# Kernel tuning notes

Hardware: AMD Instinct MI355X
Metric: run time of the kernel (lower is better)

The kernel has to match this reference:

```python
import jax, jax.numpy as jnp
import numpy as np

PI = float(np.pi)


def setup_inputs() -> dict:
    key = jax.random.key(0)
    k1, k2 = jax.random.split(key)
    src = jax.random.normal(k1, (32, 4, 512, 512), dtype=jnp.float32)
    fc2 = jax.random.normal(k2, (32, 7), dtype=jnp.float32)
    return {"src": src, "fc2": fc2}


def _build_mat(fc2):
    # Parameter extraction exactly as in the torch module.
    theta = jnp.clip(fc2[:, 0] * 0.3, -1.0, 1.0) * PI          # rotation angle
    scale = jnp.clip(fc2[:, 1:3] * 0.3 + 1.0, 0.0, 5.0)
    trans = fc2[:, 3:5] * 0.3
    shear = jnp.clip(fc2[:, 5:7] * 0.3, -1.0, 1.0) * PI
    sx, sy = scale[:, 0], scale[:, 1]
    tx, ty = trans[:, 0], trans[:, 1]
    shxy, shyx = shear[:, 0], shear[:, 1]
    c, s = jnp.cos(theta), jnp.sin(theta)
    z, o = jnp.zeros_like(c), jnp.ones_like(c)

    def m3(rows):  # rows: list of 3 lists of 3 (B,) scalars -> (B,3,3)
        return jnp.stack([jnp.stack(r, axis=-1) for r in rows], axis=-2)

    # Note: the torch code stacks rows at dim=2 (making the transpose) then
    # transposes (1,2) back, so the effective matrices are the ones as-written.
    rot = m3([[c, -s, z], [s, c, z], [z, z, o]])
    scl = m3([[sx, z, z], [z, sy, z], [z, z, o]])
    shr = m3([[o, shxy, z], [shyx, o, z], [z, z, o]])
    trn = m3([[o, z, tx], [z, o, ty], [z, z, o]])
    # mat = T @ Sh @ S @ R  (batched 3x3 matmuls)
    return trn @ shr @ scl @ rot


def _affine_grid(theta2x3, H, W):
    # F.affine_grid with align_corners=False (the torch default used here):
    # pixel centers map to x=(2w+1)/W-1, y=(2h+1)/H-1.
    xs = (2.0 * jnp.arange(W, dtype=jnp.float32) + 1.0) / W - 1.0  # (W,)
    ys = (2.0 * jnp.arange(H, dtype=jnp.float32) + 1.0) / H - 1.0  # (H,)
    base = jnp.stack([
        jnp.broadcast_to(xs[None, :], (H, W)),
        jnp.broadcast_to(ys[:, None], (H, W)),
        jnp.ones((H, W), dtype=jnp.float32),
    ], axis=-1)                                                     # (H,W,3)
    return jnp.einsum('bij,hwj->bhwi', theta2x3, base)              # (B,H,W,2)


def _grid_sample(src, grid):
    # bilinear, padding_mode='zeros', align_corners=False
    B, C, H, W = src.shape
    ix = ((grid[..., 0] + 1.0) * W - 1.0) * 0.5  # (B,H,W) source x coords
    iy = ((grid[..., 1] + 1.0) * H - 1.0) * 0.5
    x0 = jnp.floor(ix)
    y0 = jnp.floor(iy)
    wx = ix - x0  # frac weights
    wy = iy - y0
    x0i = x0.astype(jnp.int32)
    y0i = y0.astype(jnp.int32)

    def gather(img, xi, yi):  # img (C,H,W); xi,yi (H,W) int
        valid = ((xi >= 0) & (xi < W) & (yi >= 0) & (yi < H)).astype(img.dtype)
        v = img[:, jnp.clip(yi, 0, H - 1), jnp.clip(xi, 0, W - 1)]  # (C,H,W)
        return v * valid[None]

    def per_batch(img, x0i, y0i, wx, wy):
        v00 = gather(img, x0i, y0i)
        v01 = gather(img, x0i + 1, y0i)
        v10 = gather(img, x0i, y0i + 1)
        v11 = gather(img, x0i + 1, y0i + 1)
        return (v00 * (1 - wx) * (1 - wy) + v01 * wx * (1 - wy)
                + v10 * (1 - wx) * wy + v11 * wx * wy)

    return jax.vmap(per_batch)(src, x0i, y0i, wx, wy)


def reference(src, fc2):
    H, W = src.shape[2], src.shape[3]
    mat = _build_mat(fc2)                     # (B,3,3)
    inv_mat = jnp.linalg.inv(mat)             # (B,3,3)
    grid = _affine_grid(mat[:, :2, :], H, W)
    inv_grid = _affine_grid(inv_mat[:, :2, :], H, W)
    transformed = _grid_sample(src, grid)
    return transformed, mat, inv_mat, grid, inv_grid
```

## Files before the change

kernel.cpp:

```cpp
#include <hip/hip_runtime.h>
#include <hip/hip_bf16.h>

#define PI_F 3.14159265358979323846f

typedef float f32x2 __attribute__((ext_vector_type(2)));

__global__ void build_mats_kernel(const float* __restrict__ fc2,
                                  float* __restrict__ mat_out,
                                  float* __restrict__ inv_out,
                                  int B) {
    int b = blockIdx.x * blockDim.x + threadIdx.x;
    if (b >= B) return;
    const float* f = fc2 + b * 7;
    float theta = fminf(fmaxf(f[0] * 0.3f, -1.f), 1.f) * PI_F;
    float sx    = fminf(fmaxf(f[1] * 0.3f + 1.f, 0.f), 5.f);
    float sy    = fminf(fmaxf(f[2] * 0.3f + 1.f, 0.f), 5.f);
    float tx    = f[3] * 0.3f;
    float ty    = f[4] * 0.3f;
    float shxy  = fminf(fmaxf(f[5] * 0.3f, -1.f), 1.f) * PI_F;
    float shyx  = fminf(fmaxf(f[6] * 0.3f, -1.f), 1.f) * PI_F;

    float c = cosf(theta), s = sinf(theta);
    float m00 =  sx * c + shxy * sy * s;
    float m01 = -sx * s + shxy * sy * c;
    float m02 = tx;
    float m10 = shyx * sx * c + sy * s;
    float m11 = -shyx * sx * s + sy * c;
    float m12 = ty;

    float* m = mat_out + b * 9;
    m[0] = m00; m[1] = m01; m[2] = m02;
    m[3] = m10; m[4] = m11; m[5] = m12;
    m[6] = 0.f; m[7] = 0.f; m[8] = 1.f;

    float det = m00 * m11 - m01 * m10;
    float id  = 1.f / det;
    float i00 =  m11 * id, i01 = -m01 * id;
    float i10 = -m10 * id, i11 =  m00 * id;
    float i02 = -(i00 * m02 + i01 * m12);
    float i12 = -(i10 * m02 + i11 * m12);

    float* im = inv_out + b * 9;
    im[0] = i00; im[1] = i01; im[2] = i02;
    im[3] = i10; im[4] = i11; im[5] = i12;
    im[6] = 0.f; im[7] = 0.f; im[8] = 1.f;
}

__global__ __launch_bounds__(256) void affine_main_kernel(
    const float* __restrict__ src,
    const float* __restrict__ mat,
    const float* __restrict__ inv_mat,
    float* __restrict__ transformed,
    float* __restrict__ grid_out,
    float* __restrict__ inv_grid_out)
{
    const int W = 512, H = 512, C = 4;
    const int tx = threadIdx.x;
    const int ty = threadIdx.y;
    const int tz = threadIdx.z;
    const int w = blockIdx.x * 16 + (tz & 1) * 8 + tx;
    const int h = blockIdx.y * 16 + (tz >> 1) * 8 + ty;
    const int b = blockIdx.z;

    float xs = (2.f * (float)w + 1.f) * (1.f / (float)W) - 1.f;
    float ys = (2.f * (float)h + 1.f) * (1.f / (float)H) - 1.f;

    const float* m  = mat + b * 9;
    const float* im = inv_mat + b * 9;
    float gx  = m[0] * xs + m[1] * ys + m[2];
    float gy  = m[3] * xs + m[4] * ys + m[5];
    float igx = im[0] * xs + im[1] * ys + im[2];
    float igy = im[3] * xs + im[4] * ys + im[5];

    size_t pix = ((size_t)b * H + h) * W + w;
    f32x2 g2  = {gx, gy};
    f32x2 ig2 = {igx, igy};
    __builtin_nontemporal_store(g2,  (f32x2*)grid_out + pix);
    __builtin_nontemporal_store(ig2, (f32x2*)inv_grid_out + pix);

    float ix = ((gx + 1.f) * (float)W - 1.f) * 0.5f;
    float iy = ((gy + 1.f) * (float)H - 1.f) * 0.5f;
    float x0f = floorf(ix), y0f = floorf(iy);
    float wx = ix - x0f, wy = iy - y0f;
    int x0 = (int)x0f, y0 = (int)y0f;
    int x1 = x0 + 1,   y1 = y0 + 1;

    bool vx0 = (x0 >= 0) && (x0 < W);
    bool vx1 = (x1 >= 0) && (x1 < W);
    bool vy0 = (y0 >= 0) && (y0 < H);
    bool vy1 = (y1 >= 0) && (y1 < H);
    int cx0 = min(max(x0, 0), W - 1), cx1 = min(max(x1, 0), W - 1);
    int cy0 = min(max(y0, 0), H - 1), cy1 = min(max(y1, 0), H - 1);

    float w00 = (1.f - wx) * (1.f - wy) * ((vx0 && vy0) ? 1.f : 0.f);
    float w01 = wx * (1.f - wy)         * ((vx1 && vy0) ? 1.f : 0.f);
    float w10 = (1.f - wx) * wy         * ((vx0 && vy1) ? 1.f : 0.f);
    float w11 = wx * wy                 * ((vx1 && vy1) ? 1.f : 0.f);

    const float* sb = src + (size_t)b * C * H * W;
    int o00 = cy0 * W + cx0;
    int o01 = cy0 * W + cx1;
    int o10 = cy1 * W + cx0;
    int o11 = cy1 * W + cx1;

    #pragma unroll
    for (int c = 0; c < C; ++c) {
        const float* sc = sb + c * (H * W);
        float v = sc[o00] * w00 + sc[o01] * w01 + sc[o10] * w10 + sc[o11] * w11;
        transformed[(((size_t)b * C + c) * H + h) * W + w] = v;
    }
}

extern "C" void kernel_launch(void* const* d_in, const int* in_sizes, int n_in,
                              void* d_out, int out_size, void* d_ws, size_t ws_size,
                              hipStream_t stream) {
    const float* src = (const float*)d_in[0];
    const float* fc2 = (const float*)d_in[1];

    const int B = 32, C = 4, H = 512, W = 512;
    float* out = (float*)d_out;

    float* transformed  = out;
    float* mat_out      = out + (size_t)B * C * H * W;
    float* inv_out      = mat_out + (size_t)B * 9;
    float* grid_out     = inv_out + (size_t)B * 9;
    float* inv_grid_out = grid_out + (size_t)B * H * W * 2;

    build_mats_kernel<<<1, 64, 0, stream>>>(fc2, mat_out, inv_out, B);

    dim3 grid(W / 16, H / 16, B);
    dim3 block(8, 8, 4);
    affine_main_kernel<<<grid, block, 0, stream>>>(src, mat_out, inv_out,
                                                   transformed, grid_out, inv_grid_out);
}
```

Measured before the change: 460.6 us.

## Split grid writing into separate vectorized kernel and reshape sampling blocks

Moves the grid and inverse-grid output writes out of the sampling kernel into a dedicated kernel that computes two pixels per thread and stores 16-byte vectors per row. The sampling kernel now recomputes only the forward grid, uses 16-wide rows for coalescing, and writes transformed output with nontemporal stores. This trades an extra kernel launch for wider stores and a lighter gather kernel.

```diff
diff --git a/kernel.cpp b/kernel.cpp
--- a/kernel.cpp
+++ b/kernel.cpp
@@ -1,9 +1,8 @@
 #include <hip/hip_runtime.h>
-#include <hip/hip_bf16.h>
 
 #define PI_F 3.14159265358979323846f
 
-typedef float f32x2 __attribute__((ext_vector_type(2)));
+typedef float f32x4 __attribute__((ext_vector_type(4)));
 
 __global__ void build_mats_kernel(const float* __restrict__ fc2,
                                   float* __restrict__ mat_out,
@@ -46,37 +45,56 @@
     im[6] = 0.f; im[7] = 0.f; im[8] = 1.f;
 }
 
-__global__ __launch_bounds__(256) void affine_main_kernel(
-    const float* __restrict__ src,
+__global__ __launch_bounds__(256) void grid_kernel(
     const float* __restrict__ mat,
     const float* __restrict__ inv_mat,
-    float* __restrict__ transformed,
     float* __restrict__ grid_out,
     float* __restrict__ inv_grid_out)
 {
+    const int W = 512, H = 512;
+    const int h = blockIdx.x;
+    const int b = blockIdx.y;
+    const int w = threadIdx.x * 2;
+
+    float xs0 = (2.f * (float)w + 1.f) * (1.f / (float)W) - 1.f;
+    float xs1 = xs0 + 2.f / (float)W;
+    float ys  = (2.f * (float)h + 1.f) * (1.f / (float)H) - 1.f;
+
+    const float* m  = mat + b * 9;
+    const float* im = inv_mat + b * 9;
+
+    float gx0  = m[0] * xs0 + (m[1] * ys + m[2]);
+    float gy0  = m[3] * xs0 + (m[4] * ys + m[5]);
+    float gx1  = m[0] * xs1 + (m[1] * ys + m[2]);
+    float gy1  = m[3] * xs1 + (m[4] * ys + m[5]);
+    float igx0 = im[0] * xs0 + (im[1] * ys + im[2]);
+    float igy0 = im[3] * xs0 + (im[4] * ys + im[5]);
+    float igx1 = im[0] * xs1 + (im[1] * ys + im[2]);
+    float igy1 = im[3] * xs1 + (im[4] * ys + im[5]);
+
+    size_t vec = ((size_t)b * H + h) * (W / 2) + threadIdx.x;
+    f32x4 g  = {gx0, gy0, gx1, gy1};
+    f32x4 ig = {igx0, igy0, igx1, igy1};
+    __builtin_nontemporal_store(g,  (f32x4*)grid_out + vec);
+    __builtin_nontemporal_store(ig, (f32x4*)inv_grid_out + vec);
+}
+
+__global__ __launch_bounds__(256) void sample_kernel(
+    const float* __restrict__ src,
+    const float* __restrict__ mat,
+    float* __restrict__ transformed)
+{
     const int W = 512, H = 512, C = 4;
-    const int tx = threadIdx.x;
-    const int ty = threadIdx.y;
-    const int tz = threadIdx.z;
-    const int w = blockIdx.x * 16 + (tz & 1) * 8 + tx;
-    const int h = blockIdx.y * 16 + (tz >> 1) * 8 + ty;
+    const int w = blockIdx.x * 16 + threadIdx.x;
+    const int h = blockIdx.y * 16 + threadIdx.z * 4 + threadIdx.y;
     const int b = blockIdx.z;
 
     float xs = (2.f * (float)w + 1.f) * (1.f / (float)W) - 1.f;
     float ys = (2.f * (float)h + 1.f) * (1.f / (float)H) - 1.f;
 
-    const float* m  = mat + b * 9;
-    const float* im = inv_mat + b * 9;
-    float gx  = m[0] * xs + m[1] * ys + m[2];
-    float gy  = m[3] * xs + m[4] * ys + m[5];
-    float igx = im[0] * xs + im[1] * ys + im[2];
-    float igy = im[3] * xs + im[4] * ys + im[5];
-
-    size_t pix = ((size_t)b * H + h) * W + w;
-    f32x2 g2  = {gx, gy};
-    f32x2 ig2 = {igx, igy};
-    __builtin_nontemporal_store(g2,  (f32x2*)grid_out + pix);
-    __builtin_nontemporal_store(ig2, (f32x2*)inv_grid_out + pix);
+    const float* m = mat + b * 9;
+    float gx = m[0] * xs + (m[1] * ys + m[2]);
+    float gy = m[3] * xs + (m[4] * ys + m[5]);
 
     float ix = ((gx + 1.f) * (float)W - 1.f) * 0.5f;
     float iy = ((gy + 1.f) * (float)H - 1.f) * 0.5f;
@@ -107,7 +125,8 @@
     for (int c = 0; c < C; ++c) {
         const float* sc = sb + c * (H * W);
         float v = sc[o00] * w00 + sc[o01] * w01 + sc[o10] * w10 + sc[o11] * w11;
-        transformed[(((size_t)b * C + c) * H + h) * W + w] = v;
+        __builtin_nontemporal_store(
+            v, transformed + (((size_t)b * C + c) * H + h) * W + w);
     }
 }
 
@@ -128,8 +147,9 @@
 
     build_mats_kernel<<<1, 64, 0, stream>>>(fc2, mat_out, inv_out, B);
 
-    dim3 grid(W / 16, H / 16, B);
-    dim3 block(8, 8, 4);
-    affine_main_kernel<<<grid, block, 0, stream>>>(src, mat_out, inv_out,
-                                                   transformed, grid_out, inv_grid_out);
+    grid_kernel<<<dim3(H, B), 256, 0, stream>>>(mat_out, inv_out,
+                                                grid_out, inv_grid_out);
+
+    sample_kernel<<<dim3(W / 16, H / 16, B), dim3(16, 4, 4), 0, stream>>>(
+        src, mat_out, transformed);
 }
```

New measurement: 445.7 us. 3.2% less time.
